# Kernel optimization log

Hardware: AMD Instinct MI355X
Metric: run time of the kernel (lower is better)

The kernel has to match this reference:

```python
import jax, jax.numpy as jnp
import numpy as np

S, IN_DIM = 16384, 1024
NUM_PROJ, PROJ_DIM, BINS = 100, 64, 20
D = NUM_PROJ * PROJ_DIM
EPS = 1e-12  # F.normalize eps


def setup_inputs() -> dict:
    key = jax.random.key(0)
    kx, kw = jax.random.split(key)
    x = jax.random.normal(kx, (S, IN_DIM), dtype=jnp.float32)
    W = jax.random.normal(kw, (D, IN_DIM), dtype=jnp.float32)  # nn.Linear weight, std=1.0 init
    # mins/maxs as produced by cal_min_max over the data (per projected dim)
    proj = x @ W.T
    mins = jnp.min(proj, axis=0)
    maxs = jnp.max(proj, axis=0)
    return {"x": x, "W": W, "mins": mins, "maxs": maxs,
            "num_of_projection": NUM_PROJ, "bins": BINS}


def reference(x, W, mins, maxs, num_of_projection, bins):
    # get_global_feature(x, normalize=True), all histograms fused via scatter-add
    proj = x @ W.T                                   # [S, D]
    d = proj.shape[1]
    proj_dim = d // num_of_projection
    width = maxs - mins                              # [D]
    # torch.histc semantics: values in [min, max] counted; value == max -> last bin
    idx = jnp.floor((proj - mins) / width * bins).astype(jnp.int32)
    idx = jnp.clip(idx, 0, bins - 1)
    valid = (proj >= mins) & (proj <= maxs)
    flat = idx + jnp.arange(d, dtype=jnp.int32)[None, :] * bins   # [S, D]
    hist = jnp.zeros(d * bins, dtype=proj.dtype).at[flat.reshape(-1)].add(
        valid.reshape(-1).astype(proj.dtype))
    gv = hist.reshape(num_of_projection, proj_dim, bins)
    # F.normalize(p=2, dim=2)
    norm = jnp.linalg.norm(gv, axis=2, keepdims=True)
    gv = gv / jnp.maximum(norm, EPS)
    return gv
```

## Files before the change

kernel.cpp:

```cpp
#include <hip/hip_runtime.h>
#include <cmath>

#define S_DIM 16384
#define K_DIM 1024
#define D_DIM 6400
#define NBINS 20
#define HSTRIDE 21

using half_t = _Float16;
using half8  = __attribute__((ext_vector_type(8))) _Float16;
using f32x4  = __attribute__((ext_vector_type(4))) float;

__global__ void cvt_f32_f16(const float* __restrict__ a, half_t* __restrict__ da, int n8a,
                            const float* __restrict__ b, half_t* __restrict__ db, int n8b,
                            float4* __restrict__ z, int nz4) {
  int i = blockIdx.x * blockDim.x + threadIdx.x;
  if (i < nz4) z[i] = (float4){0.f, 0.f, 0.f, 0.f};
  const float* s; half_t* d; int idx;
  if (i < n8a) { s = a; d = da; idx = i; }
  else { idx = i - n8a; if (idx >= n8b) return; s = b; d = db; }
  float4 v0 = ((const float4*)s)[idx * 2];
  float4 v1 = ((const float4*)s)[idx * 2 + 1];
  half8 h = { (half_t)v0.x, (half_t)v0.y, (half_t)v0.z, (half_t)v0.w,
              (half_t)v1.x, (half_t)v1.y, (half_t)v1.z, (half_t)v1.w };
  ((half8*)d)[idx] = h;
}

#define VMWAIT(N) __asm__ volatile("s_waitcnt vmcnt(" #N ")" ::: "memory")
#define BAR()     __asm__ volatile("s_barrier" ::: "memory")
#define SP1()     __builtin_amdgcn_s_setprio(1)
#define SP0()     __builtin_amdgcn_s_setprio(0)

#define GLL(SRC, DST) __builtin_amdgcn_global_load_lds(                      \
    (const __attribute__((address_space(1))) void*)(SRC),                    \
    (__attribute__((address_space(3))) void*)(DST), 16, 0, 0)

__global__ __launch_bounds__(1024, 4) void gemm_hist256(
    const half_t* __restrict__ xh, const half_t* __restrict__ wh,
    const float* __restrict__ mins, const float* __restrict__ maxs,
    int* __restrict__ ghist)
{
  __shared__ __align__(16) char ldsA[2 * 16384];
  __shared__ __align__(16) char ldsB[2 * 16384];
  __shared__ int shist[256 * HSTRIDE];

  const int t    = threadIdx.x;
  const int lane = t & 63;
  const int wv   = t >> 6;
  const int wm   = wv >> 2;
  const int wn   = wv & 3;
  const int l16  = lane & 15;
  const int quad = lane >> 4;

  const int bid = blockIdx.x;
  const int wg  = (bid & 7) * 200 + (bid >> 3);
  const int ct  = wg / 64;
  const int rt  = wg - ct * 64;
  const int colBase = ct * 256;
  const int rowBase = rt * 256;

  for (int i = t; i < 256 * HSTRIDE; i += 1024) shist[i] = 0;

  const int swz = (quad ^ ((l16 >> 1) & 3)) * 16;
  const char* pA = ldsA + (wm * 64 + l16) * 64 + swz;
  const char* pB = ldsB + (wn * 64 + l16) * 64 + swz;

  const int r0   = t >> 2;
  const int gOff = r0 * K_DIM + (((t & 3) ^ ((t >> 3) & 3)) * 8);
  const int wvD  = wv * 1024;

  const half_t* xS = xh + (size_t)rowBase * K_DIM + gOff;
  const half_t* wS = wh + (size_t)colBase * K_DIM + gOff;

  f32x4 acc[4][4];
#pragma unroll
  for (int m = 0; m < 4; ++m)
#pragma unroll
    for (int n = 0; n < 4; ++n) acc[m][n] = (f32x4){0.f, 0.f, 0.f, 0.f};

  half8 aLo[2], aHi[2], bLo[2], bHi[2];

#define MFMA4(AH, BH, MO, NO)                                                \
  _Pragma("unroll") for (int m2 = 0; m2 < 2; ++m2)                           \
  _Pragma("unroll") for (int n2 = 0; n2 < 2; ++n2)                           \
    acc[(MO) + m2][(NO) + n2] = __builtin_amdgcn_mfma_f32_16x16x32_f16(      \
        AH[m2], BH[n2], acc[(MO) + m2][(NO) + n2], 0, 0, 0);

  GLL(xS,      ldsA + wvD);
  GLL(wS,      ldsB + wvD);
  GLL(xS + 32, ldsA + 16384 + wvD);
  GLL(wS + 32, ldsB + 16384 + wvD);
  VMWAIT(2); BAR();
  aLo[0] = *(const half8*)(pA);  aLo[1] = *(const half8*)(pA + 1024);
  bLo[0] = *(const half8*)(pB);  bLo[1] = *(const half8*)(pB + 1024);

  const half_t* xStg = xS + 64;
  const half_t* wStg = wS + 64;

#define TILE(PB, PN, RDA, RDB, STG, W1A)                                     \
  {                                                                          \
    bHi[0] = *(const half8*)(pB + (PB) + 2048);                              \
    bHi[1] = *(const half8*)(pB + (PB) + 3072);                              \
    SP1(); MFMA4(aLo, bLo, 0, 0); SP0();                                     \
    aHi[0] = *(const half8*)(pA + (PB) + 2048);                              \
    aHi[1] = *(const half8*)(pA + (PB) + 3072);                              \
    SP1(); MFMA4(aLo, bHi, 0, 2); SP0();                                     \
    W1A; BAR();                                                              \
    if (RDA) {                                                               \
      aLo[0] = *(const half8*)(pA + (PN));                                   \
      aLo[1] = *(const half8*)(pA + (PN) + 1024);                            \
    }                                                                        \
    SP1(); MFMA4(aHi, bHi, 2, 2); SP0();                                     \
    VMWAIT(0); BAR();                                                        \
    if (STG) {                                                               \
      GLL(xStg, ldsA + (PB) + wvD);                                          \
      GLL(wStg, ldsB + (PB) + wvD);                                          \
      xStg += 32; wStg += 32;                                                \
    }                                                                        \
    SP1(); MFMA4(aHi, bLo, 2, 0); SP0();                                     \
    if (RDB) {                                                               \
      bLo[0] = *(const half8*)(pB + (PN));                                   \
      bLo[1] = *(const half8*)(pB + (PN) + 1024);                            \
    }                                                                        \
  }

#pragma unroll 1
  for (int it = 0; it < 15; ++it) {
    TILE(0,     16384, 1, 1, 1, VMWAIT(1));
    TILE(16384, 0,     1, 1, 1, VMWAIT(1));
  }
  TILE(0,     16384, 1, 1, 0, VMWAIT(1));
  TILE(16384, 0,     0, 0, 0, VMWAIT(0));

#undef TILE

#pragma unroll
  for (int nf = 0; nf < 4; ++nf) {
    const int lc = wn * 64 + nf * 16 + l16;
    const float a = mins[colBase + lc], b = maxs[colBase + lc];
    const float sc = (float)NBINS / (b - a);
    int* colHist = &shist[lc * HSTRIDE];
#pragma unroll
    for (int mf = 0; mf < 4; ++mf) {
#pragma unroll
      for (int r = 0; r < 4; ++r) {
        float v = acc[mf][nf][r];
        if (v >= a && v <= b) {
          int bin = (int)((v - a) * sc);
          bin = bin > NBINS - 1 ? NBINS - 1 : bin;
          atomicAdd(&colHist[bin], 1);
        }
      }
    }
  }
  __syncthreads();
  for (int i = t; i < 256 * NBINS; i += 1024) {
    int col = i / NBINS, bin = i - col * NBINS;
    int v = shist[col * HSTRIDE + bin];
    if (v) atomicAdd(&ghist[colBase * NBINS + i], v);
  }
}

__global__ __launch_bounds__(256) void gemm_hist_fb(
    const float* __restrict__ xf, const float* __restrict__ wf,
    const float* __restrict__ mins, const float* __restrict__ maxs,
    int* __restrict__ ghist)
{
  __shared__ __align__(16) half_t ldsA[4096];
  __shared__ __align__(16) half_t ldsB[4096];
  __shared__ int shist[128 * HSTRIDE];

  const int t     = threadIdx.x;
  const int lane  = t & 63;
  const int wv    = t >> 6;
  const int waveM = wv >> 1;
  const int waveN = wv & 1;
  const int l16   = lane & 15;
  const int quad  = lane >> 4;
  const int colBase = blockIdx.x * 128;

  for (int i = t; i < 128 * HSTRIDE; i += 256) shist[i] = 0;

  float mn[4], mx[4], inv[4];
  int lcol[4];
#pragma unroll
  for (int nt = 0; nt < 4; ++nt) {
    int lc = waveN * 64 + nt * 16 + l16;
    lcol[nt] = lc;
    float a = mins[colBase + lc], b = maxs[colBase + lc];
    mn[nt] = a; mx[nt] = b;
    inv[nt] = (float)NBINS / (b - a);
  }

  int aOff[4], bOff[4];
#pragma unroll
  for (int mt = 0; mt < 4; ++mt) {
    int m = waveM * 64 + mt * 16 + l16;
    aOff[mt] = (m * 4 + (quad ^ ((m >> 1) & 3))) * 8;
  }
#pragma unroll
  for (int nt = 0; nt < 4; ++nt) {
    int n = waveN * 64 + nt * 16 + l16;
    bOff[nt] = (n * 4 + (quad ^ ((n >> 1) & 3))) * 8;
  }

  for (int rt = blockIdx.y; rt < S_DIM / 128; rt += gridDim.y) {
    const int rowBase = rt * 128;
    f32x4 acc[4][4];
#pragma unroll
    for (int mt = 0; mt < 4; ++mt)
#pragma unroll
      for (int nt = 0; nt < 4; ++nt) acc[mt][nt] = (f32x4){0.f, 0.f, 0.f, 0.f};

    for (int kt = 0; kt < K_DIM; kt += 32) {
      __syncthreads();
#pragma unroll
      for (int i = 0; i < 2; ++i) {
        const int seg = t + i * 256;
        const int row = seg >> 2;
        const int kch = (seg & 3) ^ ((row >> 1) & 3);
        const float* ga = xf + (size_t)(rowBase + row) * K_DIM + kt + kch * 8;
        float4 v0 = ((const float4*)ga)[0];
        float4 v1 = ((const float4*)ga)[1];
        half8 h = { (half_t)v0.x, (half_t)v0.y, (half_t)v0.z, (half_t)v0.w,
                    (half_t)v1.x, (half_t)v1.y, (half_t)v1.z, (half_t)v1.w };
        *(half8*)&ldsA[seg * 8] = h;
        const float* gb = wf + (size_t)(colBase + row) * K_DIM + kt + kch * 8;
        float4 u0 = ((const float4*)gb)[0];
        float4 u1 = ((const float4*)gb)[1];
        half8 g = { (half_t)u0.x, (half_t)u0.y, (half_t)u0.z, (half_t)u0.w,
                    (half_t)u1.x, (half_t)u1.y, (half_t)u1.z, (half_t)u1.w };
        *(half8*)&ldsB[seg * 8] = g;
      }
      __syncthreads();
      {
        half8 aFf[4], bFf[4];
#pragma unroll
        for (int mt = 0; mt < 4; ++mt) aFf[mt] = *(const half8*)&ldsA[aOff[mt]];
#pragma unroll
        for (int nt = 0; nt < 4; ++nt) bFf[nt] = *(const half8*)&ldsB[bOff[nt]];
#pragma unroll
        for (int mt = 0; mt < 4; ++mt)
#pragma unroll
          for (int nt = 0; nt < 4; ++nt)
            acc[mt][nt] = __builtin_amdgcn_mfma_f32_16x16x32_f16(
                aFf[mt], bFf[nt], acc[mt][nt], 0, 0, 0);
      }
    }

#pragma unroll
    for (int nt = 0; nt < 4; ++nt) {
      const float a = mn[nt], b = mx[nt], sc = inv[nt];
      int* colHist = &shist[lcol[nt] * HSTRIDE];
#pragma unroll
      for (int mt = 0; mt < 4; ++mt) {
#pragma unroll
        for (int r = 0; r < 4; ++r) {
          float v = acc[mt][nt][r];
          if (v >= a && v <= b) {
            int bin = (int)((v - a) * sc);
            bin = bin > NBINS - 1 ? NBINS - 1 : bin;
            atomicAdd(&colHist[bin], 1);
          }
        }
      }
    }
  }

  __syncthreads();
  for (int i = t; i < 128 * NBINS; i += 256) {
    int col = i / NBINS, bin = i - col * NBINS;
    int v = shist[col * HSTRIDE + bin];
    if (v) atomicAdd(&ghist[colBase * NBINS + i], v);
  }
}

__global__ void normalize_kernel(const int* __restrict__ hist, float* __restrict__ out) {
  int g = blockIdx.x * blockDim.x + threadIdx.x;
  if (g >= D_DIM) return;
  const int base = g * NBINS;
  float v[NBINS];
  float ss = 0.f;
#pragma unroll
  for (int i = 0; i < NBINS; ++i) { v[i] = (float)hist[base + i]; ss += v[i] * v[i]; }
  float sc = 1.0f / fmaxf(sqrtf(ss), 1e-12f);
#pragma unroll
  for (int i = 0; i < NBINS; ++i) out[base + i] = v[i] * sc;
}

extern "C" void kernel_launch(void* const* d_in, const int* in_sizes, int n_in,
                              void* d_out, int out_size, void* d_ws, size_t ws_size,
                              hipStream_t stream) {
  const float* x    = (const float*)d_in[0];
  const float* W    = (const float*)d_in[1];
  const float* mins = (const float*)d_in[2];
  const float* maxs = (const float*)d_in[3];
  float* out = (float*)d_out;

  const size_t xh_elems = (size_t)S_DIM * K_DIM;
  const size_t wh_elems = (size_t)D_DIM * K_DIM;
  const size_t need = (xh_elems + wh_elems) * sizeof(half_t);

  if (ws_size >= need) {
    half_t* xh = (half_t*)d_ws;
    half_t* wh = xh + xh_elems;
    int n8x = (int)(xh_elems / 8), n8w = (int)(wh_elems / 8);
    int tot = n8x + n8w;
    cvt_f32_f16<<<(tot + 255) / 256, 256, 0, stream>>>(
        x, xh, n8x, W, wh, n8w, (float4*)d_out, out_size / 4);
    gemm_hist256<<<dim3(1600), 1024, 0, stream>>>(xh, wh, mins, maxs, (int*)d_out);
  } else {
    hipMemsetAsync(d_out, 0, (size_t)out_size * sizeof(float), stream);
    gemm_hist_fb<<<dim3(D_DIM / 128, 64), 256, 0, stream>>>(
        x, W, mins, maxs, (int*)d_out);
  }

  normalize_kernel<<<(D_DIM + 255) / 256, 256, 0, stream>>>((int*)d_out, out);
}
```

Before: 371.0 us.

## Double K-tile depth to 64 with 128-byte swizzled LDS rows and simpler pipeline

Each main-loop stage now stages 64 K-elements instead of 32, doubling the LDS buffers to 64KB per operand and switching to a 128-byte row layout with an 8-way XOR swizzle. The finer interleaved fragment loads and staggered wait/barrier schedule are replaced by bulk loads of all A/B fragments followed by 16 MFMAs twice per tile, with one full vmcnt(0) wait and one barrier per tile. This halves the number of barriers and loop iterations. The cost is much higher LDS use (about 150KB with the histogram), which may limit occupancy, and less overlap of LDS reads with MFMA.

```diff
diff --git a/kernel.cpp b/kernel.cpp
--- a/kernel.cpp
+++ b/kernel.cpp
@@ -26,7 +26,7 @@
   ((half8*)d)[idx] = h;
 }
 
-#define VMWAIT(N) __asm__ volatile("s_waitcnt vmcnt(" #N ")" ::: "memory")
+#define VMWAIT0() __asm__ volatile("s_waitcnt vmcnt(0)" ::: "memory")
 #define BAR()     __asm__ volatile("s_barrier" ::: "memory")
 #define SP1()     __builtin_amdgcn_s_setprio(1)
 #define SP0()     __builtin_amdgcn_s_setprio(0)
@@ -40,8 +40,8 @@
     const float* __restrict__ mins, const float* __restrict__ maxs,
     int* __restrict__ ghist)
 {
-  __shared__ __align__(16) char ldsA[2 * 16384];
-  __shared__ __align__(16) char ldsB[2 * 16384];
+  __shared__ __align__(16) char ldsA[2 * 32768];
+  __shared__ __align__(16) char ldsB[2 * 32768];
   __shared__ int shist[256 * HSTRIDE];
 
   const int t    = threadIdx.x;
@@ -61,12 +61,12 @@
 
   for (int i = t; i < 256 * HSTRIDE; i += 1024) shist[i] = 0;
 
-  const int swz = (quad ^ ((l16 >> 1) & 3)) * 16;
-  const char* pA = ldsA + (wm * 64 + l16) * 64 + swz;
-  const char* pB = ldsB + (wn * 64 + l16) * 64 + swz;
-
-  const int r0   = t >> 2;
-  const int gOff = r0 * K_DIM + (((t & 3) ^ ((t >> 3) & 3)) * 8);
+  const char* pA0 = ldsA + (wm * 64 + l16) * 128 + (((0 + quad) ^ (l16 & 7)) * 16);
+  const char* pA1 = ldsA + (wm * 64 + l16) * 128 + (((4 + quad) ^ (l16 & 7)) * 16);
+  const char* pB0 = ldsB + (wn * 64 + l16) * 128 + (((0 + quad) ^ (l16 & 7)) * 16);
+  const char* pB1 = ldsB + (wn * 64 + l16) * 128 + (((4 + quad) ^ (l16 & 7)) * 16);
+
+  const int gOff = (t >> 3) * K_DIM + (((t & 7) ^ ((t >> 3) & 7)) * 8);
   const int wvD  = wv * 1024;
 
   const half_t* xS = xh + (size_t)rowBase * K_DIM + gOff;
@@ -78,59 +78,52 @@
 #pragma unroll
     for (int n = 0; n < 4; ++n) acc[m][n] = (f32x4){0.f, 0.f, 0.f, 0.f};
 
-  half8 aLo[2], aHi[2], bLo[2], bHi[2];
-
-#define MFMA4(AH, BH, MO, NO)                                                \
-  _Pragma("unroll") for (int m2 = 0; m2 < 2; ++m2)                           \
-  _Pragma("unroll") for (int n2 = 0; n2 < 2; ++n2)                           \
-    acc[(MO) + m2][(NO) + n2] = __builtin_amdgcn_mfma_f32_16x16x32_f16(      \
-        AH[m2], BH[n2], acc[(MO) + m2][(NO) + n2], 0, 0, 0);
-
-  GLL(xS,      ldsA + wvD);
-  GLL(wS,      ldsB + wvD);
-  GLL(xS + 32, ldsA + 16384 + wvD);
-  GLL(wS + 32, ldsB + 16384 + wvD);
-  VMWAIT(2); BAR();
-  aLo[0] = *(const half8*)(pA);  aLo[1] = *(const half8*)(pA + 1024);
-  bLo[0] = *(const half8*)(pB);  bLo[1] = *(const half8*)(pB + 1024);
+  half8 aF[4], bF[4];
+
+#define MFMA16()                                                             \
+  _Pragma("unroll") for (int mf = 0; mf < 4; ++mf)                           \
+  _Pragma("unroll") for (int nf = 0; nf < 4; ++nf)                           \
+    acc[mf][nf] = __builtin_amdgcn_mfma_f32_16x16x32_f16(                    \
+        aF[mf], bF[nf], acc[mf][nf], 0, 0, 0);
+
+  GLL(xS,          ldsA + wvD);
+  GLL(xS + 131072, ldsA + 16384 + wvD);
+  GLL(wS,          ldsB + wvD);
+  GLL(wS + 131072, ldsB + 16384 + wvD);
+  VMWAIT0(); BAR();
 
   const half_t* xStg = xS + 64;
   const half_t* wStg = wS + 64;
 
-#define TILE(PB, PN, RDA, RDB, STG, W1A)                                     \
+#define TILE(PB, PN, STG)                                                    \
   {                                                                          \
-    bHi[0] = *(const half8*)(pB + (PB) + 2048);                              \
-    bHi[1] = *(const half8*)(pB + (PB) + 3072);                              \
-    SP1(); MFMA4(aLo, bLo, 0, 0); SP0();                                     \
-    aHi[0] = *(const half8*)(pA + (PB) + 2048);                              \
-    aHi[1] = *(const half8*)(pA + (PB) + 3072);                              \
-    SP1(); MFMA4(aLo, bHi, 0, 2); SP0();                                     \
-    W1A; BAR();                                                              \
-    if (RDA) {                                                               \
-      aLo[0] = *(const half8*)(pA + (PN));                                   \
-      aLo[1] = *(const half8*)(pA + (PN) + 1024);                            \
+    if (STG) {                                                               \
+      GLL(xStg,          ldsA + (PN) + wvD);                                 \
+      GLL(xStg + 131072, ldsA + (PN) + 16384 + wvD);                         \
+      GLL(wStg,          ldsB + (PN) + wvD);                                 \
+      GLL(wStg + 131072, ldsB + (PN) + 16384 + wvD);                         \
+      xStg += 64; wStg += 64;                                                \
     }                                                                        \
-    SP1(); MFMA4(aHi, bHi, 2, 2); SP0();                                     \
-    VMWAIT(0); BAR();                                                        \
-    if (STG) {                                                               \
-      GLL(xStg, ldsA + (PB) + wvD);                                          \
-      GLL(wStg, ldsB + (PB) + wvD);                                          \
-      xStg += 32; wStg += 32;                                                \
-    }                                                                        \
-    SP1(); MFMA4(aHi, bLo, 2, 0); SP0();                                     \
-    if (RDB) {                                                               \
-      bLo[0] = *(const half8*)(pB + (PN));                                   \
-      bLo[1] = *(const half8*)(pB + (PN) + 1024);                            \
-    }                                                                        \
+    _Pragma("unroll") for (int mf = 0; mf < 4; ++mf)                         \
+      aF[mf] = *(const half8*)(pA0 + (PB) + mf * 2048);                      \
+    _Pragma("unroll") for (int nf = 0; nf < 4; ++nf)                         \
+      bF[nf] = *(const half8*)(pB0 + (PB) + nf * 2048);                      \
+    SP1(); MFMA16(); SP0();                                                  \
+    _Pragma("unroll") for (int mf = 0; mf < 4; ++mf)                         \
+      aF[mf] = *(const half8*)(pA1 + (PB) + mf * 2048);                      \
+    _Pragma("unroll") for (int nf = 0; nf < 4; ++nf)                         \
+      bF[nf] = *(const half8*)(pB1 + (PB) + nf * 2048);                      \
+    SP1(); MFMA16(); SP0();                                                  \
+    VMWAIT0(); BAR();                                                        \
   }
 
 #pragma unroll 1
-  for (int it = 0; it < 15; ++it) {
-    TILE(0,     16384, 1, 1, 1, VMWAIT(1));
-    TILE(16384, 0,     1, 1, 1, VMWAIT(1));
-  }
-  TILE(0,     16384, 1, 1, 0, VMWAIT(1));
-  TILE(16384, 0,     0, 0, 0, VMWAIT(0));
+  for (int it = 0; it < 7; ++it) {
+    TILE(0,     32768, 1);
+    TILE(32768, 0,     1);
+  }
+  TILE(0,     32768, 1);
+  TILE(32768, 0,     0);
 
 #undef TILE
 
```

Result: no change. 366.6 us (-1.2%).
